# Optimization experiments

Hardware: AMD Instinct MI355X
Metric: run time of the kernel (lower is better)

## Reference

```python
import jax, jax.numpy as jnp
import numpy as np

N, C, D = 32768, 2048, 512

def setup_inputs() -> dict:
    key = jax.random.key(0)
    k1, k2, k3 = jax.random.split(key, 3)
    X = jax.random.normal(k1, (N, D), dtype=jnp.float32)
    muK = jax.random.normal(k2, (C, D), dtype=jnp.float32)
    # counts per class; zeros mark 'unvisited' classes exercising the masking path
    cK = jax.random.randint(k3, (C,), 0, 3).astype(jnp.float32)
    return {"X": X, "muK": muK, "cK": cK}

def reference(X, muK, cK):
    # find_dists(A=muK, B=X): dist[i, j] = sum_d (muK[j, d] - X[i, d])**2, scores = -dist
    # avoids materializing the N x C x D broadcast intermediate of the original).
    x2 = jnp.sum(X * X, axis=1, keepdims=True)          # (N, 1)
    m2 = jnp.sum(muK * muK, axis=1)                     # (C,)
    scores = -(x2 + m2[None, :] - 2.0 * (X @ muK.T))    # (N, C)
    # unvisited classes (cK == 0) get per-row min score minus 1
    min_col = jnp.min(scores, axis=1, keepdims=True) - 1.0  # (N, 1)
    scores = jnp.where((cK == 0.0)[None, :], min_col, scores)
    # predict(..., return_probas=True) as used in evaluate_
    return jax.nn.softmax(scores, axis=1)
```

## Files before the change

kernel.cpp:

```cpp
#include <hip/hip_runtime.h>
#include <cfloat>

#define N_ROWS 32768
#define N_CLS  2048
#define DIM    512

typedef __attribute__((ext_vector_type(8))) short short8;
typedef __attribute__((ext_vector_type(4))) short short4v;
typedef __attribute__((ext_vector_type(4))) float f32x4;

__device__ __forceinline__ unsigned f2bf_bits(float x) {
    union { float f; unsigned u; } a; a.f = x;
    return (a.u + 0x7fffu + ((a.u >> 16) & 1u)) >> 16;
}
__device__ __forceinline__ float bf_to_f(unsigned bits) {
    union { unsigned u; float f; } a; a.u = bits << 16;
    return a.f;
}
__device__ __forceinline__ void split_bf(float x, short &h, short &l) {
    unsigned hb = f2bf_bits(x);
    h = (short)hb;
    float r = x - bf_to_f(hb);
    l = (short)f2bf_bits(r);
}

__global__ __launch_bounds__(256) void split_kernel(const float* __restrict__ src,
                                                    short* __restrict__ hi,
                                                    short* __restrict__ lo) {
    int idx = blockIdx.x * 256 + threadIdx.x;
    float4 v = ((const float4*)src)[idx];
    short h0, h1, h2, h3, l0, l1, l2, l3;
    split_bf(v.x, h0, l0); split_bf(v.y, h1, l1);
    split_bf(v.z, h2, l2); split_bf(v.w, h3, l3);
    ((short4v*)hi)[idx] = (short4v){h0, h1, h2, h3};
    ((short4v*)lo)[idx] = (short4v){l0, l1, l2, l3};
}

__global__ __launch_bounds__(256) void m2_kernel(const float* __restrict__ muK,
                                                 float* __restrict__ m2) {
    const int j = blockIdx.x;
    const int t = threadIdx.x;
    const float* r = muK + (size_t)j * DIM;
    float a = r[t], b = r[t + 256];
    float s = a * a + b * b;
    for (int off = 32; off; off >>= 1) s += __shfl_xor(s, off);
    __shared__ float sw[4];
    if ((t & 63) == 0) sw[t >> 6] = s;
    __syncthreads();
    if (t == 0) m2[j] = sw[0] + sw[1] + sw[2] + sw[3];
}

#define GLDS16(g, l) __builtin_amdgcn_global_load_lds( \
    (const __attribute__((address_space(1))) unsigned int*)(g), \
    (__attribute__((address_space(3))) unsigned int*)(l), 16, 0, 0)

__global__ __launch_bounds__(512, 2) void gemm_kernel(const short* __restrict__ Xh,
                                                      const short* __restrict__ Xl,
                                                      const short* __restrict__ Mh,
                                                      const short* __restrict__ Ml,
                                                      const float* __restrict__ m2,
                                                      float* __restrict__ S) {
    __shared__ __align__(16) short Ash[2][256 * 32];
    __shared__ __align__(16) short Asl[2][256 * 32];
    __shared__ __align__(16) short Bsh[2][256 * 32];
    __shared__ __align__(16) short Bsl[2][256 * 32];

    const int tid = threadIdx.x;

    const int bid = blockIdx.y * gridDim.x + blockIdx.x;
    const int swb = (bid & 7) * 128 + (bid >> 3);
    const int n0  = (swb & 7) * 256;
    const int m0  = (swb >> 3) * 256;

    const int w    = tid >> 6;
    const int lane = tid & 63;
    const int wrow = (w >> 2) * 128;
    const int wcol = (w & 3) * 64;
    const int l16  = lane & 15;
    const int quad = lane >> 4;

    const int q0 = tid;
    const int q1 = tid + 512;
    const size_t ga0 = (size_t)(m0 + (q0 >> 2)) * DIM + (size_t)(((q0 & 3) ^ ((q0 >> 3) & 3)) * 8);
    const size_t ga1 = (size_t)(m0 + (q1 >> 2)) * DIM + (size_t)(((q1 & 3) ^ ((q1 >> 3) & 3)) * 8);
    const size_t gb0 = (size_t)(n0 + (q0 >> 2)) * DIM + (size_t)(((q0 & 3) ^ ((q0 >> 3) & 3)) * 8);
    const size_t gb1 = (size_t)(n0 + (q1 >> 2)) * DIM + (size_t)(((q1 & 3) ^ ((q1 >> 3) & 3)) * 8);

    const int sw = (quad ^ ((l16 >> 1) & 3)) * 8;

#define STAGE(B, KK) do { \
        GLDS16(Xh + ga0 + (KK), &Ash[B][q0 * 8]); \
        GLDS16(Xh + ga1 + (KK), &Ash[B][q1 * 8]); \
        GLDS16(Xl + ga0 + (KK), &Asl[B][q0 * 8]); \
        GLDS16(Xl + ga1 + (KK), &Asl[B][q1 * 8]); \
        GLDS16(Mh + gb0 + (KK), &Bsh[B][q0 * 8]); \
        GLDS16(Mh + gb1 + (KK), &Bsh[B][q1 * 8]); \
        GLDS16(Ml + gb0 + (KK), &Bsl[B][q0 * 8]); \
        GLDS16(Ml + gb1 + (KK), &Bsl[B][q1 * 8]); \
    } while (0)

    f32x4 acc[8][4];
#pragma unroll
    for (int mt = 0; mt < 8; ++mt)
#pragma unroll
        for (int nt = 0; nt < 4; ++nt)
            acc[mt][nt] = (f32x4){0.f, 0.f, 0.f, 0.f};

    STAGE(0, 0);

#pragma unroll 1
    for (int kt = 0; kt < 16; ++kt) {
        const int cur = kt & 1;
        if (kt < 15) {
            STAGE(cur ^ 1, (kt + 1) * 32);
            asm volatile("s_waitcnt vmcnt(8)" ::: "memory");
        } else {
            asm volatile("s_waitcnt vmcnt(0)" ::: "memory");
        }
        __builtin_amdgcn_s_barrier();

        short8 ah[8], al[8];
#pragma unroll
        for (int mt = 0; mt < 8; ++mt) {
            const int ro = (wrow + mt * 16 + l16) * 32 + sw;
            ah[mt] = *(const short8*)&Ash[cur][ro];
            al[mt] = *(const short8*)&Asl[cur][ro];
        }
#pragma unroll
        for (int nt = 0; nt < 4; ++nt) {
            const int ro = (wcol + nt * 16 + l16) * 32 + sw;
            short8 bh = *(const short8*)&Bsh[cur][ro];
            short8 bl = *(const short8*)&Bsl[cur][ro];
#pragma unroll
            for (int mt = 0; mt < 8; ++mt)
                acc[mt][nt] = __builtin_amdgcn_mfma_f32_16x16x32_bf16(ah[mt], bh, acc[mt][nt], 0, 0, 0);
#pragma unroll
            for (int mt = 0; mt < 8; ++mt)
                acc[mt][nt] = __builtin_amdgcn_mfma_f32_16x16x32_bf16(ah[mt], bl, acc[mt][nt], 0, 0, 0);
#pragma unroll
            for (int mt = 0; mt < 8; ++mt)
                acc[mt][nt] = __builtin_amdgcn_mfma_f32_16x16x32_bf16(al[mt], bh, acc[mt][nt], 0, 0, 0);
        }

        __builtin_amdgcn_s_barrier();
    }
#undef STAGE

#pragma unroll
    for (int nt = 0; nt < 4; ++nt) {
        int col = n0 + wcol + nt * 16 + l16;
        float mm = m2[col];
#pragma unroll
        for (int mt = 0; mt < 8; ++mt) {
            int rbase = m0 + wrow + mt * 16 + quad * 4;
#pragma unroll
            for (int r = 0; r < 4; ++r)
                S[(size_t)(rbase + r) * N_CLS + col] = 2.0f * acc[mt][nt][r] - mm;
        }
    }
}

#define LDR 40
__global__ __launch_bounds__(256) void gemm_fallback(const float* __restrict__ X,
                                                     const float* __restrict__ muK,
                                                     const float* __restrict__ m2,
                                                     float* __restrict__ S) {
    __shared__ __align__(16) short Ah[128 * LDR];
    __shared__ __align__(16) short Al[128 * LDR];
    __shared__ __align__(16) short Bh[128 * LDR];
    __shared__ __align__(16) short Bl[128 * LDR];
    const int tid  = threadIdx.x;
    const int n0   = blockIdx.x * 128;
    const int m0   = blockIdx.y * 128;
    const int w    = tid >> 6;
    const int lane = tid & 63;
    const int wm   = (w >> 1) * 64;
    const int wn   = (w & 1) * 64;
    const int l16  = lane & 15;
    const int quad = lane >> 4;
    f32x4 acc[4][4];
#pragma unroll
    for (int mt = 0; mt < 4; ++mt)
#pragma unroll
        for (int nt = 0; nt < 4; ++nt)
            acc[mt][nt] = (f32x4){0.f, 0.f, 0.f, 0.f};
    for (int kt = 0; kt < DIM; kt += 32) {
        __syncthreads();
#pragma unroll
        for (int i = 0; i < 4; ++i) {
            int idx = tid + 256 * i;
            int row = idx >> 3;
            int c4  = (idx & 7) * 4;
            float4 fa = *(const float4*)(X + (size_t)(m0 + row) * DIM + kt + c4);
            float4 fb = *(const float4*)(muK + (size_t)(n0 + row) * DIM + kt + c4);
            short h0, h1, h2, h3, l0, l1, l2, l3;
            split_bf(fa.x, h0, l0); split_bf(fa.y, h1, l1);
            split_bf(fa.z, h2, l2); split_bf(fa.w, h3, l3);
            *(short4v*)&Ah[row * LDR + c4] = (short4v){h0, h1, h2, h3};
            *(short4v*)&Al[row * LDR + c4] = (short4v){l0, l1, l2, l3};
            split_bf(fb.x, h0, l0); split_bf(fb.y, h1, l1);
            split_bf(fb.z, h2, l2); split_bf(fb.w, h3, l3);
            *(short4v*)&Bh[row * LDR + c4] = (short4v){h0, h1, h2, h3};
            *(short4v*)&Bl[row * LDR + c4] = (short4v){l0, l1, l2, l3};
        }
        __syncthreads();
        short8 ah[4], al[4];
#pragma unroll
        for (int mt = 0; mt < 4; ++mt) {
            int r = wm + mt * 16 + l16;
            ah[mt] = *(const short8*)&Ah[r * LDR + quad * 8];
            al[mt] = *(const short8*)&Al[r * LDR + quad * 8];
        }
#pragma unroll
        for (int nt = 0; nt < 4; ++nt) {
            int r = wn + nt * 16 + l16;
            short8 bh = *(const short8*)&Bh[r * LDR + quad * 8];
            short8 bl = *(const short8*)&Bl[r * LDR + quad * 8];
#pragma unroll
            for (int mt = 0; mt < 4; ++mt)
                acc[mt][nt] = __builtin_amdgcn_mfma_f32_16x16x32_bf16(ah[mt], bh, acc[mt][nt], 0, 0, 0);
#pragma unroll
            for (int mt = 0; mt < 4; ++mt)
                acc[mt][nt] = __builtin_amdgcn_mfma_f32_16x16x32_bf16(ah[mt], bl, acc[mt][nt], 0, 0, 0);
#pragma unroll
            for (int mt = 0; mt < 4; ++mt)
                acc[mt][nt] = __builtin_amdgcn_mfma_f32_16x16x32_bf16(al[mt], bh, acc[mt][nt], 0, 0, 0);
        }
    }
#pragma unroll
    for (int nt = 0; nt < 4; ++nt) {
        int col = n0 + wn + nt * 16 + l16;
        float mm = m2[col];
#pragma unroll
        for (int mt = 0; mt < 4; ++mt) {
            int rbase = m0 + wm + mt * 16 + quad * 4;
#pragma unroll
            for (int r = 0; r < 4; ++r)
                S[(size_t)(rbase + r) * N_CLS + col] = 2.0f * acc[mt][nt][r] - mm;
        }
    }
}

__device__ __forceinline__ void sm_load_row(float* S, int row, int lane, f32x4* v) {
    const f32x4* pi = (const f32x4*)(S + (size_t)row * N_CLS);
#pragma unroll
    for (int i = 0; i < 8; ++i) v[i] = pi[i * 64 + lane];
}

__device__ __forceinline__ void sm_compute_store(float* S, int row, int lane,
                                                 unsigned msk, f32x4* v) {
    float mn = FLT_MAX, mx = -FLT_MAX;
#pragma unroll
    for (int i = 0; i < 8; ++i) {
        f32x4 s = v[i];
        mn = fminf(mn, fminf(fminf(s.x, s.y), fminf(s.z, s.w)));
        if (!((msk >> (i * 4 + 0)) & 1u)) mx = fmaxf(mx, s.x);
        if (!((msk >> (i * 4 + 1)) & 1u)) mx = fmaxf(mx, s.y);
        if (!((msk >> (i * 4 + 2)) & 1u)) mx = fmaxf(mx, s.z);
        if (!((msk >> (i * 4 + 3)) & 1u)) mx = fmaxf(mx, s.w);
    }
    for (int off = 32; off; off >>= 1) {
        mn = fminf(mn, __shfl_xor(mn, off));
        mx = fmaxf(mx, __shfl_xor(mx, off));
    }
    if (mx == -FLT_MAX) mx = mn - 1.0f;
    const float fill = mn - 1.0f;

    float sum = 0.f;
#pragma unroll
    for (int i = 0; i < 8; ++i) {
        f32x4 s = v[i];
        s.x = __expf(((msk >> (i * 4 + 0)) & 1u ? fill : s.x) - mx);
        s.y = __expf(((msk >> (i * 4 + 1)) & 1u ? fill : s.y) - mx);
        s.z = __expf(((msk >> (i * 4 + 2)) & 1u ? fill : s.z) - mx);
        s.w = __expf(((msk >> (i * 4 + 3)) & 1u ? fill : s.w) - mx);
        sum += s.x + s.y + s.z + s.w;
        v[i] = s;
    }
    for (int off = 32; off; off >>= 1) sum += __shfl_xor(sum, off);
    const float inv = 1.0f / sum;
    f32x4* po = (f32x4*)(S + (size_t)row * N_CLS);
#pragma unroll
    for (int i = 0; i < 8; ++i) {
        f32x4 s = v[i] * inv;
        __builtin_nontemporal_store(s, &po[i * 64 + lane]);
    }
}

__global__ __launch_bounds__(256) void softmax_kernel(float* __restrict__ S,
                                                      const float* __restrict__ cK) {
    const int w    = threadIdx.x >> 6;
    const int lane = threadIdx.x & 63;
    const float4* ck4 = (const float4*)cK;

    unsigned msk = 0;
#pragma unroll
    for (int i = 0; i < 8; ++i) {
        float4 k = ck4[i * 64 + lane];
        if (k.x == 0.f) msk |= 1u << (i * 4 + 0);
        if (k.y == 0.f) msk |= 1u << (i * 4 + 1);
        if (k.z == 0.f) msk |= 1u << (i * 4 + 2);
        if (k.w == 0.f) msk |= 1u << (i * 4 + 3);
    }

    const int r0 = blockIdx.x * 16 + w * 4;
    f32x4 va[8], vb[8];

    sm_load_row(S, r0 + 0, lane, va);
    sm_load_row(S, r0 + 1, lane, vb);
    sm_compute_store(S, r0 + 0, lane, msk, va);
    sm_load_row(S, r0 + 2, lane, va);
    sm_compute_store(S, r0 + 1, lane, msk, vb);
    sm_load_row(S, r0 + 3, lane, vb);
    sm_compute_store(S, r0 + 2, lane, msk, va);
    sm_compute_store(S, r0 + 3, lane, msk, vb);
}

extern "C" void kernel_launch(void* const* d_in, const int* in_sizes, int n_in,
                              void* d_out, int out_size, void* d_ws, size_t ws_size,
                              hipStream_t stream) {
    const float* X   = (const float*)d_in[0];
    const float* muK = (const float*)d_in[1];
    const float* cK  = (const float*)d_in[2];
    float* out = (float*)d_out;

    const size_t XN = (size_t)N_ROWS * DIM;
    const size_t MN = (size_t)N_CLS * DIM;
    const size_t need = (2 * XN + 2 * MN) * sizeof(short) + N_CLS * sizeof(float);

    if (ws_size >= need) {
        short* Xh = (short*)d_ws;
        short* Xl = Xh + XN;
        short* Mh = Xl + XN;
        short* Ml = Mh + MN;
        float* m2 = (float*)(Ml + MN);
        split_kernel<<<(int)(XN / 4 / 256), 256, 0, stream>>>(X, Xh, Xl);
        split_kernel<<<(int)(MN / 4 / 256), 256, 0, stream>>>(muK, Mh, Ml);
        m2_kernel<<<N_CLS, 256, 0, stream>>>(muK, m2);
        dim3 grid256(N_CLS / 256, N_ROWS / 256);
        gemm_kernel<<<grid256, 512, 0, stream>>>(Xh, Xl, Mh, Ml, m2, out);
    } else {
        float* m2f = (float*)d_ws;
        m2_kernel<<<N_CLS, 256, 0, stream>>>(muK, m2f);
        dim3 grid128(N_CLS / 128, N_ROWS / 128);
        gemm_fallback<<<grid128, 256, 0, stream>>>(X, muK, m2f, out);
    }
    softmax_kernel<<<N_ROWS / 16, 256, 0, stream>>>(out, cK);
}
```

Baseline: 560.1 us.

## Interleave split-bf16 MFMA phases with staggered global-to-LDS prefetch and setprio

Restructures the GEMM main loop into four phases of two M-tiles each. The next stage's global-to-LDS loads are spread across the phases, one operand per phase, and each phase's MFMAs are issued under s_setprio(1) with barriers between phases, in the style of a ping-pong schedule. The goal is to overlap LDS reads and global traffic with matrix-core work more evenly and to shrink each wave's register footprint for A fragments. In exchange it adds several block barriers per k-step and now waits with vmcnt(0) at the top of each iteration, which could expose memory latency.

```diff
diff --git a/kernel.cpp b/kernel.cpp
--- a/kernel.cpp
+++ b/kernel.cpp
@@ -88,17 +88,6 @@
 
     const int sw = (quad ^ ((l16 >> 1) & 3)) * 8;
 
-#define STAGE(B, KK) do { \
-        GLDS16(Xh + ga0 + (KK), &Ash[B][q0 * 8]); \
-        GLDS16(Xh + ga1 + (KK), &Ash[B][q1 * 8]); \
-        GLDS16(Xl + ga0 + (KK), &Asl[B][q0 * 8]); \
-        GLDS16(Xl + ga1 + (KK), &Asl[B][q1 * 8]); \
-        GLDS16(Mh + gb0 + (KK), &Bsh[B][q0 * 8]); \
-        GLDS16(Mh + gb1 + (KK), &Bsh[B][q1 * 8]); \
-        GLDS16(Ml + gb0 + (KK), &Bsl[B][q0 * 8]); \
-        GLDS16(Ml + gb1 + (KK), &Bsl[B][q1 * 8]); \
-    } while (0)
-
     f32x4 acc[8][4];
 #pragma unroll
     for (int mt = 0; mt < 8; ++mt)
@@ -106,45 +95,102 @@
         for (int nt = 0; nt < 4; ++nt)
             acc[mt][nt] = (f32x4){0.f, 0.f, 0.f, 0.f};
 
-    STAGE(0, 0);
+    GLDS16(Xh + ga0, &Ash[0][q0 * 8]);
+    GLDS16(Xh + ga1, &Ash[0][q1 * 8]);
+    GLDS16(Xl + ga0, &Asl[0][q0 * 8]);
+    GLDS16(Xl + ga1, &Asl[0][q1 * 8]);
+    GLDS16(Mh + gb0, &Bsh[0][q0 * 8]);
+    GLDS16(Mh + gb1, &Bsh[0][q1 * 8]);
+    GLDS16(Ml + gb0, &Bsl[0][q0 * 8]);
+    GLDS16(Ml + gb1, &Bsl[0][q1 * 8]);
 
 #pragma unroll 1
     for (int kt = 0; kt < 16; ++kt) {
         const int cur = kt & 1;
-        if (kt < 15) {
-            STAGE(cur ^ 1, (kt + 1) * 32);
-            asm volatile("s_waitcnt vmcnt(8)" ::: "memory");
-        } else {
-            asm volatile("s_waitcnt vmcnt(0)" ::: "memory");
-        }
+        const int nxt = cur ^ 1;
+        const int kkn = (kt + 1) * 32;
+        const bool pre = (kt < 15);
+
+        asm volatile("s_waitcnt vmcnt(0)" ::: "memory");
         __builtin_amdgcn_s_barrier();
 
-        short8 ah[8], al[8];
-#pragma unroll
-        for (int mt = 0; mt < 8; ++mt) {
-            const int ro = (wrow + mt * 16 + l16) * 32 + sw;
-            ah[mt] = *(const short8*)&Ash[cur][ro];
-            al[mt] = *(const short8*)&Asl[cur][ro];
-        }
+        short8 bh[4], bl[4];
+
 #pragma unroll
         for (int nt = 0; nt < 4; ++nt) {
             const int ro = (wcol + nt * 16 + l16) * 32 + sw;
-            short8 bh = *(const short8*)&Bsh[cur][ro];
-            short8 bl = *(const short8*)&Bsl[cur][ro];
-#pragma unroll
-            for (int mt = 0; mt < 8; ++mt)
-                acc[mt][nt] = __builtin_amdgcn_mfma_f32_16x16x32_bf16(ah[mt], bh, acc[mt][nt], 0, 0, 0);
-#pragma unroll
-            for (int mt = 0; mt < 8; ++mt)
-                acc[mt][nt] = __builtin_amdgcn_mfma_f32_16x16x32_bf16(ah[mt], bl, acc[mt][nt], 0, 0, 0);
-#pragma unroll
-            for (int mt = 0; mt < 8; ++mt)
-                acc[mt][nt] = __builtin_amdgcn_mfma_f32_16x16x32_bf16(al[mt], bh, acc[mt][nt], 0, 0, 0);
-        }
-
-        __builtin_amdgcn_s_barrier();
-    }
-#undef STAGE
+            bh[nt] = *(const short8*)&Bsh[cur][ro];
+            bl[nt] = *(const short8*)&Bsl[cur][ro];
+        }
+        {
+            const int roA = (wrow + 0 * 16 + l16) * 32 + sw;
+            const int roB = (wrow + 1 * 16 + l16) * 32 + sw;
+            short8 ahA = *(const short8*)&Ash[cur][roA];
+            short8 alA = *(const short8*)&Asl[cur][roA];
+            short8 ahB = *(const short8*)&Ash[cur][roB];
+            short8 alB = *(const short8*)&Asl[cur][roB];
+            if (pre) {
+                GLDS16(Xh + ga0 + kkn, &Ash[nxt][q0 * 8]);
+                GLDS16(Xh + ga1 + kkn, &Ash[nxt][q1 * 8]);
+            }
+            asm volatile("s_waitcnt lgkmcnt(8)" ::: "memory");
+            __builtin_amdgcn_sched_barrier(0);
+            __builtin_amdgcn_s_barrier();
+            asm volatile("s_waitcnt lgkmcnt(0)" ::: "memory");
+            __builtin_amdgcn_sched_barrier(0);
+            __builtin_amdgcn_s_setprio(1);
+#pragma unroll
+            for (int nt = 0; nt < 4; ++nt) {
+                acc[0][nt] = __builtin_amdgcn_mfma_f32_16x16x32_bf16(ahA, bh[nt], acc[0][nt], 0, 0, 0);
+                acc[1][nt] = __builtin_amdgcn_mfma_f32_16x16x32_bf16(ahB, bh[nt], acc[1][nt], 0, 0, 0);
+                acc[0][nt] = __builtin_amdgcn_mfma_f32_16x16x32_bf16(ahA, bl[nt], acc[0][nt], 0, 0, 0);
+                acc[1][nt] = __builtin_amdgcn_mfma_f32_16x16x32_bf16(ahB, bl[nt], acc[1][nt], 0, 0, 0);
+                acc[0][nt] = __builtin_amdgcn_mfma_f32_16x16x32_bf16(alA, bh[nt], acc[0][nt], 0, 0, 0);
+                acc[1][nt] = __builtin_amdgcn_mfma_f32_16x16x32_bf16(alB, bh[nt], acc[1][nt], 0, 0, 0);
+            }
+            __builtin_amdgcn_s_setprio(0);
+            __builtin_amdgcn_s_barrier();
+        }
+
+#pragma unroll
+        for (int p = 1; p < 4; ++p) {
+            const int mtA = 2 * p, mtB = 2 * p + 1;
+            const int roA = (wrow + mtA * 16 + l16) * 32 + sw;
+            const int roB = (wrow + mtB * 16 + l16) * 32 + sw;
+            short8 ahA = *(const short8*)&Ash[cur][roA];
+            short8 alA = *(const short8*)&Asl[cur][roA];
+            short8 ahB = *(const short8*)&Ash[cur][roB];
+            short8 alB = *(const short8*)&Asl[cur][roB];
+            if (pre) {
+                if (p == 1) {
+                    GLDS16(Xl + ga0 + kkn, &Asl[nxt][q0 * 8]);
+                    GLDS16(Xl + ga1 + kkn, &Asl[nxt][q1 * 8]);
+                } else if (p == 2) {
+                    GLDS16(Mh + gb0 + kkn, &Bsh[nxt][q0 * 8]);
+                    GLDS16(Mh + gb1 + kkn, &Bsh[nxt][q1 * 8]);
+                } else {
+                    GLDS16(Ml + gb0 + kkn, &Bsl[nxt][q0 * 8]);
+                    GLDS16(Ml + gb1 + kkn, &Bsl[nxt][q1 * 8]);
+                }
+            }
+            __builtin_amdgcn_sched_barrier(0);
+            __builtin_amdgcn_s_barrier();
+            asm volatile("s_waitcnt lgkmcnt(0)" ::: "memory");
+            __builtin_amdgcn_sched_barrier(0);
+            __builtin_amdgcn_s_setprio(1);
+#pragma unroll
+            for (int nt = 0; nt < 4; ++nt) {
+                acc[mtA][nt] = __builtin_amdgcn_mfma_f32_16x16x32_bf16(ahA, bh[nt], acc[mtA][nt], 0, 0, 0);
+                acc[mtB][nt] = __builtin_amdgcn_mfma_f32_16x16x32_bf16(ahB, bh[nt], acc[mtB][nt], 0, 0, 0);
+                acc[mtA][nt] = __builtin_amdgcn_mfma_f32_16x16x32_bf16(ahA, bl[nt], acc[mtA][nt], 0, 0, 0);
+                acc[mtB][nt] = __builtin_amdgcn_mfma_f32_16x16x32_bf16(ahB, bl[nt], acc[mtB][nt], 0, 0, 0);
+                acc[mtA][nt] = __builtin_amdgcn_mfma_f32_16x16x32_bf16(alA, bh[nt], acc[mtA][nt], 0, 0, 0);
+                acc[mtB][nt] = __builtin_amdgcn_mfma_f32_16x16x32_bf16(alB, bh[nt], acc[mtB][nt], 0, 0, 0);
+            }
+            __builtin_amdgcn_s_setprio(0);
+            __builtin_amdgcn_s_barrier();
+        }
+    }
 
 #pragma unroll
     for (int nt = 0; nt < 4; ++nt) {
```

New measurement: 554.8 us. About the same (-0.9%).
